# Performance work log

Measured on AMD Instinct MI355X. Metric: run time of the kernel, lower is better.

## Reference

```python
import jax, jax.numpy as jnp
import numpy as np

IN_CH = 128
OUT_CH = 128
MODES = 16
T = 32
N = 32768
SCALE = 1.0 / (IN_CH * OUT_CH)  # TIME_CONV mode


def setup_inputs() -> dict:
    key = jax.random.key(0)
    k_x, k_w = jax.random.split(key)
    x = jax.random.normal(k_x, (T, N, IN_CH), dtype=jnp.float32)
    # nn.Parameter(scale * torch.rand(in, out, modes, 2)) — real/imag stacked in last dim
    weights = SCALE * jax.random.uniform(k_w, (IN_CH, OUT_CH, MODES, 2), dtype=jnp.float32)
    return {"x": x, "weights": weights}


def reference(x, weights):
    # x: [T, N, C_in]; weights: [C_in, C_out, modes, 2]
    w_c = weights[..., 0] + 1j * weights[..., 1]           # [i, o, m] complex
    x_ft = jnp.fft.rfft(x, axis=0)                          # [T//2+1, N, C_in] complex
    out_ft = jnp.einsum('mni,iom->mno', x_ft[:MODES], w_c)  # [modes, N, C_out] complex
    out = jnp.fft.irfft(out_ft, n=T, axis=0)                # [T, N, C_out] real
    return out
```

## Files before the change

### kernel.cpp

```cpp
#include <hip/hip_runtime.h>
#include <math.h>

typedef short bf16x8 __attribute__((ext_vector_type(8)));
typedef short bf16x4 __attribute__((ext_vector_type(4)));
typedef float f32x4  __attribute__((ext_vector_type(4)));

#define TT 32
#define MM 16
#define CC 128
#define NPT 32768
#define NC 4194304
#define BN 16

#define XF_OFF   0
#define OF0_OFF  131072
#define OF1_OFF  147456
#define LDS_BYTES 163840

static __device__ __forceinline__ unsigned short f2bf(float f) {
    union { float f; unsigned u; } v; v.f = f;
    unsigned r = v.u + 0x7FFFu + ((v.u >> 16) & 1u);
    return (unsigned short)(r >> 16);
}
static __device__ __forceinline__ unsigned pack2(float lo, float hi) {
    return (unsigned)f2bf(lo) | ((unsigned)f2bf(hi) << 16);
}

__global__ void repack_w(const float* __restrict__ w, bf16x8* __restrict__ wb) {
    int r = blockIdx.x * blockDim.x + threadIdx.x;
    int lane = r & 63;
    int r2 = r >> 6;
    int ck = r2 & 7;
    int r3 = r2 >> 3;
    int ri = r3 & 1;
    int r4 = r3 >> 1;
    int og = r4 & 7;
    int m  = r4 >> 3;
    int o = og * 16 + (lane & 15);
    int kbase = ck * 32 + (lane >> 4) * 8;
    bf16x8 v;
    #pragma unroll
    for (int j = 0; j < 8; ++j) {
        int k = kbase + j;
        int i = k >> 1, ko = k & 1;
        const float* wp = w + ((size_t)(i * 128 + o) * 16 + m) * 2;
        float val;
        if (ri == 0) val = ko ? -wp[1] : wp[0];
        else         val = ko ?  wp[0] : wp[1];
        v[j] = (short)f2bf(val);
    }
    wb[r] = v;
}

__global__ __launch_bounds__(1024, 2)
void spectral_mfma(const float* __restrict__ x, const bf16x8* __restrict__ wb,
                   float* __restrict__ out) {
    extern __shared__ char lds[];
    float* tabc = (float*)(lds + OF1_OFF);
    float* tabs = (float*)(lds + OF1_OFF + 2048);
    const int tid = threadIdx.x;
    const int n0  = blockIdx.x * BN;

    const int lane = tid & 63;
    const int wid  = tid >> 6;
    const int col  = lane & 15;
    const int kq   = lane >> 4;
    const unsigned swza = (unsigned)((col & 7) << 4);
    const unsigned swzo = (unsigned)((col & 7) << 3);

    if (tid < 512) {
        int m = tid & 15, t = tid >> 4;
        float s, c;
        sincosf(0.19634954084936207f * (float)((m * t) & 31), &s, &c);
        tabc[t * 16 + m] = c;
        tabs[t * 16 + m] = s;
    }

    bf16x8 dtf0, dtf1;
    #pragma unroll
    for (int jm = 0; jm < 4; ++jm) {
        int m = kq * 4 + jm;
        float alpha = (m == 0) ? 0.03125f : 0.0625f;
        float s, c;
        sincosf(0.19634954084936207f * (float)((m * col) & 31), &s, &c);
        dtf0[jm * 2 + 0] = (short)f2bf(alpha * c);
        dtf0[jm * 2 + 1] = (m == 0) ? (short)0 : (short)f2bf(-alpha * s);
        sincosf(0.19634954084936207f * (float)((m * (col + 16)) & 31), &s, &c);
        dtf1[jm * 2 + 0] = (short)f2bf(alpha * c);
        dtf1[jm * 2 + 1] = (m == 0) ? (short)0 : (short)f2bf(-alpha * s);
    }
    __syncthreads();

    {
        const int nn = tid >> 6;
        const int i2 = (tid & 63) * 2;
        const float* xp = x + (size_t)(n0 + nn) * CC + i2;
        float2 x0  = *(const float2*)(xp);
        float2 x16 = *(const float2*)(xp + (size_t)16 * NC);
        float xrA[16], xiA[16], xrB[16], xiB[16];
        #pragma unroll
        for (int m = 0; m < 16; ++m) {
            float sgn = (m & 1) ? -1.f : 1.f;
            xrA[m] = x0.x + sgn * x16.x;
            xrB[m] = x0.y + sgn * x16.y;
            xiA[m] = 0.f; xiB[m] = 0.f;
        }
        #pragma unroll 3
        for (int t = 1; t <= 15; ++t) {
            float2 a = *(const float2*)(xp + (size_t)t * NC);
            float2 b = *(const float2*)(xp + (size_t)(32 - t) * NC);
            float ex = a.x + b.x, ey = a.y + b.y;
            float ox = a.x - b.x, oy = a.y - b.y;
            float4 c0 = *(const float4*)&tabc[t * 16 + 0];
            float4 c1 = *(const float4*)&tabc[t * 16 + 4];
            float4 c2 = *(const float4*)&tabc[t * 16 + 8];
            float4 c3 = *(const float4*)&tabc[t * 16 + 12];
            float4 s0 = *(const float4*)&tabs[t * 16 + 0];
            float4 s1 = *(const float4*)&tabs[t * 16 + 4];
            float4 s2 = *(const float4*)&tabs[t * 16 + 8];
            float4 s3 = *(const float4*)&tabs[t * 16 + 12];
            float cm[16] = {c0.x,c0.y,c0.z,c0.w, c1.x,c1.y,c1.z,c1.w,
                            c2.x,c2.y,c2.z,c2.w, c3.x,c3.y,c3.z,c3.w};
            float sm[16] = {s0.x,s0.y,s0.z,s0.w, s1.x,s1.y,s1.z,s1.w,
                            s2.x,s2.y,s2.z,s2.w, s3.x,s3.y,s3.z,s3.w};
            #pragma unroll
            for (int m = 0; m < 16; ++m) {
                xrA[m] += ex * cm[m];  xiA[m] -= ox * sm[m];
                xrB[m] += ey * cm[m];  xiB[m] -= oy * sm[m];
            }
        }
        char* xfb = lds + XF_OFF;
        const unsigned swzd = (unsigned)((nn & 7) << 4);
        #pragma unroll
        for (int m = 0; m < 16; ++m) {
            unsigned byte = ((unsigned)(m * 8192 + nn * 512 + i2 * 4)) ^ swzd;
            uint2 v2;
            v2.x = pack2(xrA[m], xiA[m]);
            v2.y = pack2(xrB[m], xiB[m]);
            *(uint2*)(xfb + byte) = v2;
        }
    }
    __syncthreads();

    char* xfb = lds + XF_OFF;
    float* outp = out + (size_t)(n0 + wid) * CC + col;
    const unsigned arow = (unsigned)(wid * 8192 + col * 512 + kq * 16);
    f32x4 sv0 = {0.f,0.f,0.f,0.f}, sv1 = {0.f,0.f,0.f,0.f};

    for (int k = 0; k <= 8; ++k) {
        if (k < 8) {
            char* ofb = lds + ((k & 1) ? OF1_OFF : OF0_OFF);
            const bf16x8* wog = wb + (size_t)((wid * 8 + k) * 2) * (8 * 64);
            f32x4 accR = {0.f, 0.f, 0.f, 0.f};
            f32x4 accI = {0.f, 0.f, 0.f, 0.f};
            #pragma unroll
            for (int ck = 0; ck < 8; ++ck) {
                bf16x8 af = *(const bf16x8*)(xfb + ((arow + (unsigned)(ck * 64)) ^ swza));
                bf16x8 bR = wog[(0 * 8 + ck) * 64 + lane];
                bf16x8 bI = wog[(1 * 8 + ck) * 64 + lane];
                accR = __builtin_amdgcn_mfma_f32_16x16x32_bf16(af, bR, accR, 0, 0, 0);
                accI = __builtin_amdgcn_mfma_f32_16x16x32_bf16(af, bI, accI, 0, 0, 0);
            }
            #pragma unroll
            for (int j = 0; j < 4; ++j) {
                unsigned no = (unsigned)((kq * 4 + j) * 16 + col);
                unsigned addr = no * 64u + (((unsigned)(wid * 4)) ^ ((no & 7) << 3));
                *(unsigned*)(ofb + addr) = pack2(accR[j], accI[j]);
            }
        }
        if (k > 0) {
            const int og = k - 1;
            char* ofb = lds + ((og & 1) ? OF1_OFF : OF0_OFF);
            unsigned rowb = (unsigned)((wid * 16 + col) * 64);
            bf16x4 lo = *(const bf16x4*)(ofb + rowb + (((unsigned)(kq * 16)) ^ swzo));
            bf16x4 hi = *(const bf16x4*)(ofb + rowb + (((unsigned)(kq * 16 + 8)) ^ swzo));
            bf16x8 pf;
            #pragma unroll
            for (int q = 0; q < 4; ++q) { pf[q] = lo[q]; pf[4 + q] = hi[q]; }
            f32x4 z = {0.f, 0.f, 0.f, 0.f};
            f32x4 c0 = __builtin_amdgcn_mfma_f32_16x16x32_bf16(dtf0, pf, z, 0, 0, 0);
            f32x4 c1 = __builtin_amdgcn_mfma_f32_16x16x32_bf16(dtf1, pf, z, 0, 0, 0);
            if ((og & 1) == 0) {
                sv0 = c0; sv1 = c1;
            } else {
                float* opE = outp + (og - 1) * 16;
                float* opO = outp + og * 16;
                #pragma unroll
                for (int j = 0; j < 4; ++j) {
                    int t0 = kq * 4 + j;
                    opE[(size_t)t0 * NC]        = sv0[j];
                    opO[(size_t)t0 * NC]        = c0[j];
                    opE[(size_t)(t0 + 16) * NC] = sv1[j];
                    opO[(size_t)(t0 + 16) * NC] = c1[j];
                }
            }
        }
        __syncthreads();
    }
}

#define FBN 8
#define FXST 36
__global__ __launch_bounds__(512, 2)
void spectral_fused(const float* __restrict__ x,
                    const float* __restrict__ w,
                    float* __restrict__ out) {
    extern __shared__ float flds[];
    float* xf    = flds;
    float* ftabc = flds + FBN * CC * FXST;
    float* ftabs = ftabc + 512;

    const int tid = threadIdx.x;
    const int n0  = blockIdx.x * FBN;

    {
        const int m = tid >> 5;
        const int t = tid & 31;
        const float ang = 0.19634954084936207f * (float)((m * t) & 31);
        float s, c; sincosf(ang, &s, &c);
        ftabc[tid] = c; ftabs[tid] = s;
    }
    __syncthreads();
    {
        const int i   = tid & 127;
        const int nnA = tid >> 7;
        const int nnB = nnA + 4;
        float xra[MM], xia[MM], xrb[MM], xib[MM];
        #pragma unroll
        for (int m = 0; m < MM; ++m) { xra[m]=0.f; xia[m]=0.f; xrb[m]=0.f; xib[m]=0.f; }
        const float* xA = x + (size_t)(n0 + nnA) * CC + i;
        const float* xB = x + (size_t)(n0 + nnB) * CC + i;
        for (int t = 0; t < TT; ++t) {
            const float va = xA[(size_t)t * NC];
            const float vb = xB[(size_t)t * NC];
            #pragma unroll
            for (int m = 0; m < MM; ++m) {
                const float c = ftabc[(m << 5) + t];
                const float s = ftabs[(m << 5) + t];
                xra[m] += va * c;  xia[m] -= va * s;
                xrb[m] += vb * c;  xib[m] -= vb * s;
            }
        }
        float* dA = xf + (size_t)(nnA * CC + i) * FXST;
        float* dB = xf + (size_t)(nnB * CC + i) * FXST;
        #pragma unroll
        for (int j = 0; j < 8; ++j) {
            *(float4*)(dA + 4 * j) = make_float4(xra[2*j], xia[2*j], xra[2*j+1], xia[2*j+1]);
            *(float4*)(dB + 4 * j) = make_float4(xrb[2*j], xib[2*j], xrb[2*j+1], xib[2*j+1]);
        }
    }
    __syncthreads();
    const int o   = tid & 127;
    const int nnA = tid >> 7;
    const int nnB = nnA + 4;
    float ar[MM], ai_[MM], br[MM], bi_[MM];
    #pragma unroll
    for (int m = 0; m < MM; ++m) { ar[m]=0.f; ai_[m]=0.f; br[m]=0.f; bi_[m]=0.f; }
    const float* qa0 = xf + (size_t)(nnA * CC) * FXST;
    const float* qb0 = xf + (size_t)(nnB * CC) * FXST;
    float4 wv[8];
    {
        const float4* wp = (const float4*)(w + (size_t)o * 32);
        #pragma unroll
        for (int j = 0; j < 8; ++j) wv[j] = wp[j];
    }
    for (int i = 0; i < CC; ++i) {
        float4 xa4[8], xb4[8];
        const float4* qa = (const float4*)(qa0 + i * FXST);
        const float4* qb = (const float4*)(qb0 + i * FXST);
        #pragma unroll
        for (int j = 0; j < 8; ++j) { xa4[j] = qa[j]; xb4[j] = qb[j]; }
        float4 wn[8];
        if (i + 1 < CC) {
            const float4* wp = (const float4*)(w + (size_t)((i + 1) * CC + o) * 32);
            #pragma unroll
            for (int j = 0; j < 8; ++j) wn[j] = wp[j];
        }
        #pragma unroll
        for (int j = 0; j < 8; ++j) {
            const int m0 = 2 * j, m1 = 2 * j + 1;
            ar[m0]  += xa4[j].x * wv[j].x - xa4[j].y * wv[j].y;
            ai_[m0] += xa4[j].x * wv[j].y + xa4[j].y * wv[j].x;
            br[m0]  += xb4[j].x * wv[j].x - xb4[j].y * wv[j].y;
            bi_[m0] += xb4[j].x * wv[j].y + xb4[j].y * wv[j].x;
            ar[m1]  += xa4[j].z * wv[j].z - xa4[j].w * wv[j].w;
            ai_[m1] += xa4[j].z * wv[j].w + xa4[j].w * wv[j].z;
            br[m1]  += xb4[j].z * wv[j].z - xb4[j].w * wv[j].w;
            bi_[m1] += xb4[j].z * wv[j].w + xb4[j].w * wv[j].z;
        }
        #pragma unroll
        for (int j = 0; j < 8; ++j) wv[j] = wn[j];
    }
    {
        const float inv = 1.0f / 32.0f;
        const size_t obA = (size_t)(n0 + nnA) * CC + o;
        const size_t obB = (size_t)(n0 + nnB) * CC + o;
        for (int t = 0; t < TT; ++t) {
            float accA = 0.f, accB = 0.f;
            #pragma unroll
            for (int m = 1; m < MM; ++m) {
                const float c = ftabc[(m << 5) + t];
                const float s = ftabs[(m << 5) + t];
                accA += ar[m] * c - ai_[m] * s;
                accB += br[m] * c - bi_[m] * s;
            }
            out[(size_t)t * NC + obA] = (ar[0] + 2.f * accA) * inv;
            out[(size_t)t * NC + obB] = (br[0] + 2.f * accB) * inv;
        }
    }
}

extern "C" void kernel_launch(void* const* d_in, const int* in_sizes, int n_in,
                              void* d_out, int out_size, void* d_ws, size_t ws_size,
                              hipStream_t stream) {
    (void)in_sizes; (void)n_in; (void)out_size;
    const float* x = (const float*)d_in[0];
    const float* w = (const float*)d_in[1];
    float* out     = (float*)d_out;

    if (d_ws != nullptr && ws_size >= (size_t)2 * 1024 * 1024) {
        bf16x8* wbuf = (bf16x8*)d_ws;
        hipLaunchKernelGGL(repack_w, dim3(512), dim3(256), 0, stream, w, wbuf);
        hipLaunchKernelGGL(spectral_mfma, dim3(NPT / BN), dim3(1024), LDS_BYTES, stream,
                           x, wbuf, out);
    } else {
        const size_t lds_bytes = (size_t)(FBN * CC * FXST + 1024) * sizeof(float);
        hipLaunchKernelGGL(spectral_fused, dim3(NPT / FBN), dim3(512), lds_bytes, stream,
                           x, w, out);
    }
}
```

Baseline: 451.5 us.

## Halve per-block node tile to shrink LDS and allow two blocks per CU

Cuts the per-block node tile from 16 to 8 and reorganises the kernel so shared memory drops from about 160KB to about 76KB. The goal is to let two 1024-thread blocks share a CU for better latency hiding on the memory-bound loads and stores. The forward DFT now handles one channel per thread instead of two. The inverse-DFT twiddles are built once in shared memory, and waves are split across the two time halves. The double-buffered spectral output is replaced by a single buffer with an extra barrier per iteration. In exchange, half of each MFMA's A rows are duplicated and a synchronisation is added per output group.

```diff
diff --git a/kernel.cpp b/kernel.cpp
--- a/kernel.cpp
+++ b/kernel.cpp
@@ -10,12 +10,12 @@
 #define CC 128
 #define NPT 32768
 #define NC 4194304
-#define BN 16
+#define BN 8
 
 #define XF_OFF   0
-#define OF0_OFF  131072
-#define OF1_OFF  147456
-#define LDS_BYTES 163840
+#define OF_OFF   65536
+#define SCR_OFF  73728
+#define LDS_BYTES 77824
 
 static __device__ __forceinline__ unsigned short f2bf(float f) {
     union { float f; unsigned u; } v; v.f = f;
@@ -56,17 +56,11 @@
 void spectral_mfma(const float* __restrict__ x, const bf16x8* __restrict__ wb,
                    float* __restrict__ out) {
     extern __shared__ char lds[];
-    float* tabc = (float*)(lds + OF1_OFF);
-    float* tabs = (float*)(lds + OF1_OFF + 2048);
+    float* tabc = (float*)(lds + SCR_OFF);
+    float* tabs = (float*)(lds + SCR_OFF + 2048);
+    char*  dtb  = lds + SCR_OFF;
     const int tid = threadIdx.x;
     const int n0  = blockIdx.x * BN;
-
-    const int lane = tid & 63;
-    const int wid  = tid >> 6;
-    const int col  = lane & 15;
-    const int kq   = lane >> 4;
-    const unsigned swza = (unsigned)((col & 7) << 4);
-    const unsigned swzo = (unsigned)((col & 7) << 3);
 
     if (tid < 512) {
         int m = tid & 15, t = tid >> 4;
@@ -75,42 +69,25 @@
         tabc[t * 16 + m] = c;
         tabs[t * 16 + m] = s;
     }
-
-    bf16x8 dtf0, dtf1;
-    #pragma unroll
-    for (int jm = 0; jm < 4; ++jm) {
-        int m = kq * 4 + jm;
-        float alpha = (m == 0) ? 0.03125f : 0.0625f;
-        float s, c;
-        sincosf(0.19634954084936207f * (float)((m * col) & 31), &s, &c);
-        dtf0[jm * 2 + 0] = (short)f2bf(alpha * c);
-        dtf0[jm * 2 + 1] = (m == 0) ? (short)0 : (short)f2bf(-alpha * s);
-        sincosf(0.19634954084936207f * (float)((m * (col + 16)) & 31), &s, &c);
-        dtf1[jm * 2 + 0] = (short)f2bf(alpha * c);
-        dtf1[jm * 2 + 1] = (m == 0) ? (short)0 : (short)f2bf(-alpha * s);
-    }
-    __syncthreads();
-
-    {
-        const int nn = tid >> 6;
-        const int i2 = (tid & 63) * 2;
-        const float* xp = x + (size_t)(n0 + nn) * CC + i2;
-        float2 x0  = *(const float2*)(xp);
-        float2 x16 = *(const float2*)(xp + (size_t)16 * NC);
-        float xrA[16], xiA[16], xrB[16], xiB[16];
+    __syncthreads();
+
+    {
+        const int nn = tid >> 7;
+        const int i  = tid & 127;
+        const float* xp = x + (size_t)(n0 + nn) * CC + i;
+        float x0  = xp[0];
+        float x16 = xp[(size_t)16 * NC];
+        float xr[16], xi[16];
         #pragma unroll
         for (int m = 0; m < 16; ++m) {
-            float sgn = (m & 1) ? -1.f : 1.f;
-            xrA[m] = x0.x + sgn * x16.x;
-            xrB[m] = x0.y + sgn * x16.y;
-            xiA[m] = 0.f; xiB[m] = 0.f;
+            xr[m] = x0 + ((m & 1) ? -x16 : x16);
+            xi[m] = 0.f;
         }
         #pragma unroll 3
         for (int t = 1; t <= 15; ++t) {
-            float2 a = *(const float2*)(xp + (size_t)t * NC);
-            float2 b = *(const float2*)(xp + (size_t)(32 - t) * NC);
-            float ex = a.x + b.x, ey = a.y + b.y;
-            float ox = a.x - b.x, oy = a.y - b.y;
+            float a = xp[(size_t)t * NC];
+            float b = xp[(size_t)(32 - t) * NC];
+            float e = a + b, od = a - b;
             float4 c0 = *(const float4*)&tabc[t * 16 + 0];
             float4 c1 = *(const float4*)&tabc[t * 16 + 4];
             float4 c2 = *(const float4*)&tabc[t * 16 + 8];
@@ -125,42 +102,71 @@
                             s2.x,s2.y,s2.z,s2.w, s3.x,s3.y,s3.z,s3.w};
             #pragma unroll
             for (int m = 0; m < 16; ++m) {
-                xrA[m] += ex * cm[m];  xiA[m] -= ox * sm[m];
-                xrB[m] += ey * cm[m];  xiB[m] -= oy * sm[m];
+                xr[m] += e * cm[m];
+                xi[m] -= od * sm[m];
             }
         }
         char* xfb = lds + XF_OFF;
         const unsigned swzd = (unsigned)((nn & 7) << 4);
         #pragma unroll
         for (int m = 0; m < 16; ++m) {
-            unsigned byte = ((unsigned)(m * 8192 + nn * 512 + i2 * 4)) ^ swzd;
-            uint2 v2;
-            v2.x = pack2(xrA[m], xiA[m]);
-            v2.y = pack2(xrB[m], xiB[m]);
-            *(uint2*)(xfb + byte) = v2;
-        }
-    }
-    __syncthreads();
+            unsigned byte = ((unsigned)(m * 4096 + nn * 512 + i * 4)) ^ swzd;
+            *(unsigned*)(xfb + byte) = pack2(xr[m], xi[m]);
+        }
+    }
+    __syncthreads();
+
+    {
+        int t = tid >> 5, k2 = tid & 31, m = k2 >> 1, ri = k2 & 1;
+        float alpha = (m == 0) ? 0.03125f : 0.0625f;
+        float s, c;
+        sincosf(0.19634954084936207f * (float)((m * t) & 31), &s, &c);
+        float val = (ri == 0) ? alpha * c : -alpha * s;
+        if (m == 0 && ri == 1) val = 0.f;
+        unsigned addr = ((unsigned)(t * 64 + k2 * 2)) ^ ((unsigned)((t & 7) << 3));
+        *(unsigned short*)(dtb + addr) = f2bf(val);
+    }
+    __syncthreads();
+
+    const int lane = tid & 63;
+    const int wid  = tid >> 6;
+    const int col  = lane & 15;
+    const int kq   = lane >> 4;
+    const int th   = wid >> 3;
+    const int nn_i = wid & 7;
+    const unsigned swza = (unsigned)((col & 7) << 4);
+    const unsigned swzo = (unsigned)((col & 7) << 3);
+    const unsigned arow = (unsigned)(wid * 4096 + (col & 7) * 512 + kq * 16);
+
+    bf16x8 dtf;
+    {
+        unsigned row = (unsigned)(th * 16 + col);
+        unsigned a0 = (row * 64u + (unsigned)(kq * 16))     ^ ((row & 7) << 3);
+        unsigned a1 = (row * 64u + (unsigned)(kq * 16 + 8)) ^ ((row & 7) << 3);
+        bf16x4 lo = *(const bf16x4*)(dtb + a0);
+        bf16x4 hi = *(const bf16x4*)(dtb + a1);
+        #pragma unroll
+        for (int q = 0; q < 4; ++q) { dtf[q] = lo[q]; dtf[4 + q] = hi[q]; }
+    }
 
     char* xfb = lds + XF_OFF;
-    float* outp = out + (size_t)(n0 + wid) * CC + col;
-    const unsigned arow = (unsigned)(wid * 8192 + col * 512 + kq * 16);
-    f32x4 sv0 = {0.f,0.f,0.f,0.f}, sv1 = {0.f,0.f,0.f,0.f};
-
-    for (int k = 0; k <= 8; ++k) {
-        if (k < 8) {
-            char* ofb = lds + ((k & 1) ? OF1_OFF : OF0_OFF);
-            const bf16x8* wog = wb + (size_t)((wid * 8 + k) * 2) * (8 * 64);
-            f32x4 accR = {0.f, 0.f, 0.f, 0.f};
-            f32x4 accI = {0.f, 0.f, 0.f, 0.f};
-            #pragma unroll
-            for (int ck = 0; ck < 8; ++ck) {
-                bf16x8 af = *(const bf16x8*)(xfb + ((arow + (unsigned)(ck * 64)) ^ swza));
-                bf16x8 bR = wog[(0 * 8 + ck) * 64 + lane];
-                bf16x8 bI = wog[(1 * 8 + ck) * 64 + lane];
-                accR = __builtin_amdgcn_mfma_f32_16x16x32_bf16(af, bR, accR, 0, 0, 0);
-                accI = __builtin_amdgcn_mfma_f32_16x16x32_bf16(af, bI, accI, 0, 0, 0);
-            }
+    char* ofb = lds + OF_OFF;
+    float* outp = out + (size_t)(n0 + nn_i) * CC + col;
+    f32x4 sv = {0.f, 0.f, 0.f, 0.f};
+
+    for (int k = 0; k < 8; ++k) {
+        const bf16x8* wog = wb + (size_t)((wid * 8 + k) * 2) * (8 * 64);
+        f32x4 accR = {0.f, 0.f, 0.f, 0.f};
+        f32x4 accI = {0.f, 0.f, 0.f, 0.f};
+        #pragma unroll
+        for (int ck = 0; ck < 8; ++ck) {
+            bf16x8 af = *(const bf16x8*)(xfb + ((arow + (unsigned)(ck * 64)) ^ swza));
+            bf16x8 bR = wog[(0 * 8 + ck) * 64 + lane];
+            bf16x8 bI = wog[(1 * 8 + ck) * 64 + lane];
+            accR = __builtin_amdgcn_mfma_f32_16x16x32_bf16(af, bR, accR, 0, 0, 0);
+            accI = __builtin_amdgcn_mfma_f32_16x16x32_bf16(af, bI, accI, 0, 0, 0);
+        }
+        if (kq < 2) {
             #pragma unroll
             for (int j = 0; j < 4; ++j) {
                 unsigned no = (unsigned)((kq * 4 + j) * 16 + col);
@@ -168,30 +174,26 @@
                 *(unsigned*)(ofb + addr) = pack2(accR[j], accI[j]);
             }
         }
-        if (k > 0) {
-            const int og = k - 1;
-            char* ofb = lds + ((og & 1) ? OF1_OFF : OF0_OFF);
-            unsigned rowb = (unsigned)((wid * 16 + col) * 64);
-            bf16x4 lo = *(const bf16x4*)(ofb + rowb + (((unsigned)(kq * 16)) ^ swzo));
-            bf16x4 hi = *(const bf16x4*)(ofb + rowb + (((unsigned)(kq * 16 + 8)) ^ swzo));
+        __syncthreads();
+        {
+            unsigned row = (unsigned)(nn_i * 16 + col);
+            bf16x4 lo = *(const bf16x4*)(ofb + row * 64u + (((unsigned)(kq * 16))     ^ swzo));
+            bf16x4 hi = *(const bf16x4*)(ofb + row * 64u + (((unsigned)(kq * 16 + 8)) ^ swzo));
             bf16x8 pf;
             #pragma unroll
             for (int q = 0; q < 4; ++q) { pf[q] = lo[q]; pf[4 + q] = hi[q]; }
             f32x4 z = {0.f, 0.f, 0.f, 0.f};
-            f32x4 c0 = __builtin_amdgcn_mfma_f32_16x16x32_bf16(dtf0, pf, z, 0, 0, 0);
-            f32x4 c1 = __builtin_amdgcn_mfma_f32_16x16x32_bf16(dtf1, pf, z, 0, 0, 0);
-            if ((og & 1) == 0) {
-                sv0 = c0; sv1 = c1;
+            f32x4 cc = __builtin_amdgcn_mfma_f32_16x16x32_bf16(dtf, pf, z, 0, 0, 0);
+            if ((k & 1) == 0) {
+                sv = cc;
             } else {
-                float* opE = outp + (og - 1) * 16;
-                float* opO = outp + og * 16;
+                float* opE = outp + (k - 1) * 16;
+                float* opO = outp + k * 16;
                 #pragma unroll
                 for (int j = 0; j < 4; ++j) {
-                    int t0 = kq * 4 + j;
-                    opE[(size_t)t0 * NC]        = sv0[j];
-                    opO[(size_t)t0 * NC]        = c0[j];
-                    opE[(size_t)(t0 + 16) * NC] = sv1[j];
-                    opO[(size_t)(t0 + 16) * NC] = c1[j];
+                    int t0 = th * 16 + kq * 4 + j;
+                    opE[(size_t)t0 * NC] = sv[j];
+                    opO[(size_t)t0 * NC] = cc[j];
                 }
             }
         }
```

Result: slower. 624.2 us (+38.3%).
